# Optimization experiments

Measured on AMD Instinct MI355X. Metric: run time of the kernel, lower is better.

Reference implementation:

```python
import jax, jax.numpy as jnp
import numpy as np

STRIDE = 1

def setup_inputs() -> dict:
    key = jax.random.key(0)
    k1, k2 = jax.random.split(key)
    x = jax.random.normal(k1, (16, 32, 32768), dtype=jnp.float32)
    # original uses torch.rand -> uniform [0,1)
    kernel = jax.random.uniform(k2, (1, 32, 32, 3), dtype=jnp.float32)
    return {"x": x, "kernel": kernel}

def reference(x, kernel):
    # Faithful intent of the module: strided valid 1D convolution.
    # x: (B, C_in, L); kernel: (1, C_out, C_in, K)
    w = kernel[0]  # (C_out, C_in, K)
    out = jax.lax.conv_general_dilated(
        x, w,
        window_strides=(STRIDE,),
        padding='VALID',
        dimension_numbers=('NCH', 'OIH', 'NCH'),
    )  # (B, C_out, (L-K)//STRIDE + 1)
    return out
```

## Files before the change

### kernel.cpp

```cpp
#include <hip/hip_runtime.h>

#define L_IN   32768
#define L_OUT  32766
#define C_IN   32
#define C_OUT  32
#define KW     3
#define TILE_L 128
#define TPB    4
#define XROWS  130
#define PITCHW 32
#define LDSW   (XROWS * PITCHW)

typedef __attribute__((ext_vector_type(8))) short bf16x8;
typedef __attribute__((ext_vector_type(4))) float f32x4;
typedef __attribute__((ext_vector_type(4))) unsigned int u32x4;

#define PIN(v_) asm volatile("" : "+v"(v_))

__device__ __forceinline__ unsigned pack_split(float v) {
    unsigned u = __float_as_uint(v);
    unsigned r = u + 0x7fffu + ((u >> 16) & 1u);
    float lo = v - __uint_as_float(r & 0xffff0000u);
    return (__float_as_uint(lo) & 0xffff0000u) | (r >> 16);
}

__device__ __forceinline__ int lds_word(int l, int ci) {
    return l * PITCHW + ((((ci >> 2) ^ (l & 7)) << 2) | (ci & 3));
}

__global__ void prep_w(const float* __restrict__ w, unsigned short* __restrict__ wtf) {
    const int i = blockIdx.x * 256 + threadIdx.x;
    if (i >= 6 * 64 * 8) return;
    const int f    = i >> 9;
    const int rr   = i & 511;
    const int lane = rr >> 3;
    const int j    = rr & 7;
    const int kw   = f >> 1;
    const int cot  = f & 1;
    const int co   = cot * 16 + (lane & 15);
    const int ci   = (lane >> 4) * 8 + j;
    const float v  = w[(co * C_IN + ci) * KW + kw];
    unsigned u = __float_as_uint(v);
    unsigned r = u + 0x7fffu + ((u >> 16) & 1u);
    unsigned short hi = (unsigned short)(r >> 16);
    float lof = v - __uint_as_float(r & 0xffff0000u);
    unsigned lu = __float_as_uint(lof);
    unsigned lr = lu + 0x7fffu + ((lu >> 16) & 1u);
    unsigned short lo = (unsigned short)(lr >> 16);
    wtf[(f * 64 + lane) * 16 + j]     = hi;
    wtf[(f * 64 + lane) * 16 + 8 + j] = lo;
}

__global__ __launch_bounds__(256, 4) void conv1d_mfma(
    const float* __restrict__ x, const unsigned short* __restrict__ wtf,
    float* __restrict__ out)
{
    __shared__ __attribute__((aligned(16))) unsigned xp[2][LDSW];

    const int tid  = threadIdx.x;
    const int lane = tid & 63;
    const int wv   = tid >> 6;
    const int bb   = blockIdx.x >> 6;
    const int grp  = blockIdx.x & 63;
    const int lg0  = grp * (TILE_L * TPB);

    const float* xb = x + (size_t)bb * C_IN * L_IN;

    u32x4 wah[6], wal[6];
#pragma unroll
    for (int f = 0; f < 6; ++f) {
        const u32x4* p = (const u32x4*)(wtf + (f * 64 + lane) * 16);
        wah[f] = p[0];
        wal[f] = p[1];
    }

    const int c   = tid & 31;
    const int rr0 = tid >> 5;
    const int n   = lane & 15;
    const int kg  = lane >> 4;
    const int lb  = wv * 32;

    float sv[4][4];
    float hv;

    auto LOADT = [&](int l0) {
#pragma unroll
        for (int r = 0; r < 4; ++r) {
            const float* src = xb + (size_t)(rr0 + r * 8) * L_IN + l0;
#pragma unroll
            for (int q = 0; q < 4; ++q)
                sv[r][q] = src[c + q * 32];
        }
        hv = 0.f;
        if (tid < 64) {
            const int gl = l0 + TILE_L + (tid & 1);
            if (gl < L_IN) hv = xb[(size_t)(tid >> 1) * L_IN + gl];
        }
        asm volatile("" ::: "memory");
    };
    auto WRITET = [&](int buf) {
        unsigned* xs = xp[buf];
#pragma unroll
        for (int r = 0; r < 4; ++r)
#pragma unroll
            for (int q = 0; q < 4; ++q)
                xs[lds_word(c + q * 32, rr0 + r * 8)] = pack_split(sv[r][q]);
        if (tid < 64)
            xs[lds_word(TILE_L + (tid & 1), tid >> 1)] = pack_split(hv);
    };

    LOADT(lg0);
    WRITET(0);
#pragma unroll
    for (int f = 0; f < 6; ++f) { PIN(wah[f]); PIN(wal[f]); }

    float* ob = out + (size_t)bb * C_OUT * L_OUT;

#pragma unroll
    for (int t = 0; t < TPB; ++t) {
        const int l0 = lg0 + t * TILE_L;
        if (t + 1 < TPB) LOADT(l0 + TILE_L);
        __syncthreads();

        const unsigned* xs = xp[t & 1];
        f32x4 acc[2][2];
#pragma unroll
        for (int a = 0; a < 2; ++a)
#pragma unroll
            for (int bq = 0; bq < 2; ++bq)
                acc[a][bq] = (f32x4){0.f, 0.f, 0.f, 0.f};

#pragma unroll
        for (int kw = 0; kw < KW; ++kw) {
#pragma unroll
            for (int lt = 0; lt < 2; ++lt) {
                const int lrow = lb + lt * 16 + n + kw;
                const int base = lrow * PITCHW;
                const int sw   = lrow & 7;
                const u32x4 pa = *(const u32x4*)&xs[base + (((kg * 2 + 0) ^ sw) << 2)];
                const u32x4 pb = *(const u32x4*)&xs[base + (((kg * 2 + 1) ^ sw) << 2)];
                u32x4 BH, BL;
                BH[0] = (pa[0] & 0xffffu) | (pa[1] << 16);
                BH[1] = (pa[2] & 0xffffu) | (pa[3] << 16);
                BH[2] = (pb[0] & 0xffffu) | (pb[1] << 16);
                BH[3] = (pb[2] & 0xffffu) | (pb[3] << 16);
                BL[0] = (pa[0] >> 16) | (pa[1] & 0xffff0000u);
                BL[1] = (pa[2] >> 16) | (pa[3] & 0xffff0000u);
                BL[2] = (pb[0] >> 16) | (pb[1] & 0xffff0000u);
                BL[3] = (pb[2] >> 16) | (pb[3] & 0xffff0000u);
                const bf16x8 bh = __builtin_bit_cast(bf16x8, BH);
                const bf16x8 bl = __builtin_bit_cast(bf16x8, BL);
#pragma unroll
                for (int cot = 0; cot < 2; ++cot) {
                    const int f = kw * 2 + cot;
                    const bf16x8 ah = __builtin_bit_cast(bf16x8, wah[f]);
                    const bf16x8 al = __builtin_bit_cast(bf16x8, wal[f]);
                    acc[cot][lt] = __builtin_amdgcn_mfma_f32_16x16x32_bf16(ah, bh, acc[cot][lt], 0, 0, 0);
                    acc[cot][lt] = __builtin_amdgcn_mfma_f32_16x16x32_bf16(ah, bl, acc[cot][lt], 0, 0, 0);
                    acc[cot][lt] = __builtin_amdgcn_mfma_f32_16x16x32_bf16(al, bh, acc[cot][lt], 0, 0, 0);
                }
            }
        }

        if (t + 1 < TPB) WRITET((t + 1) & 1);

        const int lw = l0 + lb;
        if (lw + 31 < L_OUT) {
#pragma unroll
            for (int cot = 0; cot < 2; ++cot)
#pragma unroll
                for (int lt = 0; lt < 2; ++lt) {
                    float* op = ob + (size_t)(cot * 16 + kg * 4) * L_OUT + lw + lt * 16 + n;
#pragma unroll
                    for (int r = 0; r < 4; ++r)
                        op[(size_t)r * L_OUT] = acc[cot][lt][r];
                }
        } else {
#pragma unroll
            for (int cot = 0; cot < 2; ++cot)
#pragma unroll
                for (int lt = 0; lt < 2; ++lt) {
                    const int l = lw + lt * 16 + n;
                    if (l < L_OUT) {
                        float* op = ob + (size_t)(cot * 16 + kg * 4) * L_OUT + l;
#pragma unroll
                        for (int r = 0; r < 4; ++r)
                            op[(size_t)r * L_OUT] = acc[cot][lt][r];
                    }
                }
        }
    }
}

extern "C" void kernel_launch(void* const* d_in, const int* in_sizes, int n_in,
                              void* d_out, int out_size, void* d_ws, size_t ws_size,
                              hipStream_t stream) {
    const float* x = (const float*)d_in[0];
    const float* w = (const float*)d_in[1];
    float* out     = (float*)d_out;
    unsigned short* wtf = (unsigned short*)d_ws;

    prep_w<<<dim3(12), 256, 0, stream>>>(w, wtf);
    conv1d_mfma<<<dim3(16 * 64), 256, 0, stream>>>(x, wtf, out);
}
```

Baseline: 127.8 us.

## Stage split weights in LDS, single-buffer x tile, double the grid

Split bf16 weights now sit in shared memory and are loaded per kernel tap, no longer pinned in 48 VGPRs. The x tile goes from double to single buffering with an extra barrier per iteration, and tiles per block drop from 4 to 2, so the grid doubles to 2048 blocks. The aim is lower register pressure and more parallelism for latency hiding. In exchange there are extra LDS reads for weights on every tile, a per-block weight copy, and less overlap between the global load and compute.

```diff
diff --git a/kernel.cpp b/kernel.cpp
--- a/kernel.cpp
+++ b/kernel.cpp
@@ -6,16 +6,16 @@
 #define C_OUT  32
 #define KW     3
 #define TILE_L 128
-#define TPB    4
+#define TPB    2
+#define NGRP   128
 #define XROWS  130
 #define PITCHW 32
 #define LDSW   (XROWS * PITCHW)
+#define WPLANE 3072
 
 typedef __attribute__((ext_vector_type(8))) short bf16x8;
 typedef __attribute__((ext_vector_type(4))) float f32x4;
 typedef __attribute__((ext_vector_type(4))) unsigned int u32x4;
-
-#define PIN(v_) asm volatile("" : "+v"(v_))
 
 __device__ __forceinline__ unsigned pack_split(float v) {
     unsigned u = __float_as_uint(v);
@@ -47,31 +47,32 @@
     unsigned lu = __float_as_uint(lof);
     unsigned lr = lu + 0x7fffu + ((lu >> 16) & 1u);
     unsigned short lo = (unsigned short)(lr >> 16);
-    wtf[(f * 64 + lane) * 16 + j]     = hi;
-    wtf[(f * 64 + lane) * 16 + 8 + j] = lo;
+    wtf[(f * 64 + lane) * 8 + j]          = hi;
+    wtf[WPLANE + (f * 64 + lane) * 8 + j] = lo;
 }
 
 __global__ __launch_bounds__(256, 4) void conv1d_mfma(
     const float* __restrict__ x, const unsigned short* __restrict__ wtf,
     float* __restrict__ out)
 {
-    __shared__ __attribute__((aligned(16))) unsigned xp[2][LDSW];
+    __shared__ __attribute__((aligned(16))) unsigned       xs[LDSW];
+    __shared__ __attribute__((aligned(16))) unsigned short wl[2 * WPLANE];
 
     const int tid  = threadIdx.x;
     const int lane = tid & 63;
     const int wv   = tid >> 6;
-    const int bb   = blockIdx.x >> 6;
-    const int grp  = blockIdx.x & 63;
+    const int bb   = blockIdx.x >> 7;
+    const int grp  = blockIdx.x & (NGRP - 1);
     const int lg0  = grp * (TILE_L * TPB);
 
     const float* xb = x + (size_t)bb * C_IN * L_IN;
 
-    u32x4 wah[6], wal[6];
-#pragma unroll
-    for (int f = 0; f < 6; ++f) {
-        const u32x4* p = (const u32x4*)(wtf + (f * 64 + lane) * 16);
-        wah[f] = p[0];
-        wal[f] = p[1];
+    {
+        const u32x4* wsv = (const u32x4*)wtf;
+        u32x4*       wdv = (u32x4*)wl;
+#pragma unroll
+        for (int i = 0; i < 3; ++i)
+            wdv[tid * 3 + i] = wsv[tid * 3 + i];
     }
 
     const int c   = tid & 31;
@@ -98,8 +99,7 @@
         }
         asm volatile("" ::: "memory");
     };
-    auto WRITET = [&](int buf) {
-        unsigned* xs = xp[buf];
+    auto WRITET = [&]() {
 #pragma unroll
         for (int r = 0; r < 4; ++r)
 #pragma unroll
@@ -110,19 +110,16 @@
     };
 
     LOADT(lg0);
-    WRITET(0);
-#pragma unroll
-    for (int f = 0; f < 6; ++f) { PIN(wah[f]); PIN(wal[f]); }
 
     float* ob = out + (size_t)bb * C_OUT * L_OUT;
 
 #pragma unroll
     for (int t = 0; t < TPB; ++t) {
         const int l0 = lg0 + t * TILE_L;
+        WRITET();
         if (t + 1 < TPB) LOADT(l0 + TILE_L);
         __syncthreads();
 
-        const unsigned* xs = xp[t & 1];
         f32x4 acc[2][2];
 #pragma unroll
         for (int a = 0; a < 2; ++a)
@@ -132,6 +129,11 @@
 
 #pragma unroll
         for (int kw = 0; kw < KW; ++kw) {
+            const int f0 = kw * 2, f1 = kw * 2 + 1;
+            const bf16x8 ah0 = *(const bf16x8*)&wl[(f0 * 64 + lane) * 8];
+            const bf16x8 al0 = *(const bf16x8*)&wl[WPLANE + (f0 * 64 + lane) * 8];
+            const bf16x8 ah1 = *(const bf16x8*)&wl[(f1 * 64 + lane) * 8];
+            const bf16x8 al1 = *(const bf16x8*)&wl[WPLANE + (f1 * 64 + lane) * 8];
 #pragma unroll
             for (int lt = 0; lt < 2; ++lt) {
                 const int lrow = lb + lt * 16 + n + kw;
@@ -150,19 +152,15 @@
                 BL[3] = (pb[2] >> 16) | (pb[3] & 0xffff0000u);
                 const bf16x8 bh = __builtin_bit_cast(bf16x8, BH);
                 const bf16x8 bl = __builtin_bit_cast(bf16x8, BL);
-#pragma unroll
-                for (int cot = 0; cot < 2; ++cot) {
-                    const int f = kw * 2 + cot;
-                    const bf16x8 ah = __builtin_bit_cast(bf16x8, wah[f]);
-                    const bf16x8 al = __builtin_bit_cast(bf16x8, wal[f]);
-                    acc[cot][lt] = __builtin_amdgcn_mfma_f32_16x16x32_bf16(ah, bh, acc[cot][lt], 0, 0, 0);
-                    acc[cot][lt] = __builtin_amdgcn_mfma_f32_16x16x32_bf16(ah, bl, acc[cot][lt], 0, 0, 0);
-                    acc[cot][lt] = __builtin_amdgcn_mfma_f32_16x16x32_bf16(al, bh, acc[cot][lt], 0, 0, 0);
-                }
+
+                acc[0][lt] = __builtin_amdgcn_mfma_f32_16x16x32_bf16(ah0, bh, acc[0][lt], 0, 0, 0);
+                acc[0][lt] = __builtin_amdgcn_mfma_f32_16x16x32_bf16(ah0, bl, acc[0][lt], 0, 0, 0);
+                acc[0][lt] = __builtin_amdgcn_mfma_f32_16x16x32_bf16(al0, bh, acc[0][lt], 0, 0, 0);
+                acc[1][lt] = __builtin_amdgcn_mfma_f32_16x16x32_bf16(ah1, bh, acc[1][lt], 0, 0, 0);
+                acc[1][lt] = __builtin_amdgcn_mfma_f32_16x16x32_bf16(ah1, bl, acc[1][lt], 0, 0, 0);
+                acc[1][lt] = __builtin_amdgcn_mfma_f32_16x16x32_bf16(al1, bh, acc[1][lt], 0, 0, 0);
             }
         }
-
-        if (t + 1 < TPB) WRITET((t + 1) & 1);
 
         const int lw = l0 + lb;
         if (lw + 31 < L_OUT) {
@@ -189,6 +187,8 @@
                     }
                 }
         }
+
+        if (t + 1 < TPB) __syncthreads();
     }
 }
 
@@ -201,5 +201,5 @@
     unsigned short* wtf = (unsigned short*)d_ws;
 
     prep_w<<<dim3(12), 256, 0, stream>>>(w, wtf);
-    conv1d_mfma<<<dim3(16 * 64), 256, 0, stream>>>(x, wtf, out);
-}
+    conv1d_mfma<<<dim3(16 * NGRP), 256, 0, stream>>>(x, wtf, out);
+}
```

Result: faster. 119.8 us (-6.3%).
